# Optimization experiments

Measured on AMD Instinct MI355X. Metric: run time of the kernel, lower is better.

## Reference

```python
import jax, jax.numpy as jnp
import numpy as np

EPS = 1e-12  # tf.math.l2_normalize epsilon

def _l2_normalize(v, axis):
    sq = jnp.sum(v * v, axis=axis, keepdims=True)
    return v * jax.lax.rsqrt(jnp.maximum(sq, EPS))

def setup_inputs() -> dict:
    key = jax.random.key(0)
    k1, k2, k3 = jax.random.split(key, 3)
    B, H, Wd, Cin, K = 16, 64, 64, 512, 64  # K == dim (required by the source's broadcast)
    x = jax.random.normal(k1, (B, H, Wd, Cin), dtype=jnp.float32)
    W = jax.random.normal(k2, (Cin, K), dtype=jnp.float32) * (1.0 / np.sqrt(Cin))
    b = jnp.zeros((K,), dtype=jnp.float32)
    C = jax.random.uniform(k3, (1, 1, 1, K, K), dtype=jnp.float32)  # [1,1,1,dim,clusters]
    return {"x": x, "W": W, "b": b, "C": C}

def reference(x, W, b, C):
    # 1x1 conv: per-pixel linear projection to cluster logits. NOTE: the
    # original code overwrites x with the conv output, so the VLAD residual
    # is built from these logits, not the input features (faithful to source).
    f = jnp.einsum('bhwc,ck->bhwk', x, W) + b            # [B,H,W,K]
    s = jax.nn.softmax(f, axis=-1)                        # soft assignment over clusters
    # a: [B,H,W,1,K], residual: [B,H,W,dim,K] with dim==K
    v = s[..., None, :] * (f[..., :, None] + C)           # [B,H,W,dim,K]
    v = jnp.sum(v, axis=(1, 2))                           # [B,dim,K]
    v = jnp.transpose(v, (0, 2, 1))                       # [B,K,dim]
    # postnorm=True: intra-normalize per cluster, then global L2 of flattened
    v = _l2_normalize(v, axis=-1)
    flat = v.reshape(v.shape[0], -1)                      # [B, K*dim]
    return _l2_normalize(flat, axis=-1)
```

## Files before the change

kernel.cpp:

```cpp
#include <hip/hip_runtime.h>
#include <hip/hip_bf16.h>

#define NB 16
#define HW 4096
#define CIN 512
#define KCL 64
#define BP 64
#define NCHUNK 64
#define PSTRIDE 72

typedef short s16x8 __attribute__((ext_vector_type(8)));
typedef int   i32x4 __attribute__((ext_vector_type(4)));
typedef float f32x4 __attribute__((ext_vector_type(4)));

__device__ __forceinline__ unsigned short f2bf(float f) {
    unsigned u = __builtin_bit_cast(unsigned, f);
    u += 0x7fffu + ((u >> 16) & 1u);
    return (unsigned short)(u >> 16);
}

__device__ __forceinline__ unsigned pk2(float lo, float hi) {
    __hip_bfloat162 h = __float22bfloat162_rn(make_float2(lo, hi));
    unsigned r;
    __builtin_memcpy(&r, &h, 4);
    return r;
}

__global__ void vlad_prep(const float* __restrict__ Wm, float* __restrict__ A_g,
                          unsigned short* __restrict__ Wt_g)
{
    const int i = blockIdx.x * 256 + threadIdx.x;
    if (i < NB * KCL * KCL + NB * KCL) A_g[i] = 0.f;
    if (i < CIN * KCL) {
        const int c = i >> 6;
        const int n = i & 63;
        Wt_g[n * 512 + c] = f2bf(Wm[i]);
    }
}

__global__ __launch_bounds__(256, 4) void vlad_main(
    const float* __restrict__ x, const unsigned short* __restrict__ Wt_g,
    const float* __restrict__ bv, float* __restrict__ A_g,
    float* __restrict__ sumS_g)
{
    __shared__ unsigned short ft[KCL * PSTRIDE];
    __shared__ unsigned short st[KCL * PSTRIDE];

    const int t = threadIdx.x;
    const int b = blockIdx.x >> 6;
    const int chunk = blockIdx.x & 63;
    const int pb = b * HW + chunk * BP;

    const int wid = t >> 6;
    const int lane = t & 63;
    const int col = lane & 15;
    const int g = lane >> 4;
    const int wpix = pb + wid * 16;

    f32x4 acc[4];
#pragma unroll
    for (int nt = 0; nt < 4; ++nt) acc[nt] = (f32x4){0.f, 0.f, 0.f, 0.f};

    const float* xr0 = x + (size_t)(wpix + col) * CIN + g * 8;
    const unsigned short* wbase = Wt_g + col * 512 + g * 8;

#pragma unroll
    for (int kk = 0; kk < 16; ++kk) {
        const int k0 = kk * 32;
        const float4 u00 = *(const float4*)(xr0 + k0);
        const float4 u01 = *(const float4*)(xr0 + k0 + 4);
        s16x8 wf[4];
#pragma unroll
        for (int nt = 0; nt < 4; ++nt)
            wf[nt] = *(const s16x8*)(wbase + nt * (16 * 512) + k0);
        const i32x4 a0i = {(int)pk2(u00.x, u00.y), (int)pk2(u00.z, u00.w),
                           (int)pk2(u01.x, u01.y), (int)pk2(u01.z, u01.w)};
        const s16x8 a0 = __builtin_bit_cast(s16x8, a0i);
#pragma unroll
        for (int nt = 0; nt < 4; ++nt)
            acc[nt] = __builtin_amdgcn_mfma_f32_16x16x32_bf16(a0, wf[nt], acc[nt], 0, 0, 0);
    }

    float bj[4];
#pragma unroll
    for (int nt = 0; nt < 4; ++nt) bj[nt] = bv[nt * 16 + col];
    float ssum[4] = {0.f, 0.f, 0.f, 0.f};
    float fv[4][4], sv[4][4];

#pragma unroll
    for (int r = 0; r < 4; ++r) {
        float v0 = acc[0][r] + bj[0];
        float v1 = acc[1][r] + bj[1];
        float v2 = acc[2][r] + bj[2];
        float v3 = acc[3][r] + bj[3];
        float m = fmaxf(fmaxf(v0, v1), fmaxf(v2, v3));
        m = fmaxf(m, __shfl_xor(m, 1));
        m = fmaxf(m, __shfl_xor(m, 2));
        m = fmaxf(m, __shfl_xor(m, 4));
        m = fmaxf(m, __shfl_xor(m, 8));
        const float e0 = __expf(v0 - m);
        const float e1 = __expf(v1 - m);
        const float e2 = __expf(v2 - m);
        const float e3 = __expf(v3 - m);
        float lsum = e0 + e1 + e2 + e3;
        lsum += __shfl_xor(lsum, 1);
        lsum += __shfl_xor(lsum, 2);
        lsum += __shfl_xor(lsum, 4);
        lsum += __shfl_xor(lsum, 8);
        const float rl = 1.0f / lsum;
        fv[0][r] = v0; fv[1][r] = v1; fv[2][r] = v2; fv[3][r] = v3;
        sv[0][r] = e0 * rl; sv[1][r] = e1 * rl; sv[2][r] = e2 * rl; sv[3][r] = e3 * rl;
        ssum[0] += sv[0][r]; ssum[1] += sv[1][r]; ssum[2] += sv[2][r]; ssum[3] += sv[3][r];
    }

    const int pbase = wid * 16 + g * 4;
#pragma unroll
    for (int nt = 0; nt < 4; ++nt) {
        uint2 fw, sw;
        fw.x = pk2(fv[nt][0], fv[nt][1]); fw.y = pk2(fv[nt][2], fv[nt][3]);
        sw.x = pk2(sv[nt][0], sv[nt][1]); sw.y = pk2(sv[nt][2], sv[nt][3]);
        *(uint2*)(ft + (nt * 16 + col) * PSTRIDE + pbase) = fw;
        *(uint2*)(st + (nt * 16 + col) * PSTRIDE + pbase) = sw;
    }

#pragma unroll
    for (int nt = 0; nt < 4; ++nt) {
        ssum[nt] += __shfl_xor(ssum[nt], 16);
        ssum[nt] += __shfl_xor(ssum[nt], 32);
    }
    if (g == 0) {
#pragma unroll
        for (int nt = 0; nt < 4; ++nt)
            atomicAdd(sumS_g + b * KCL + nt * 16 + col, ssum[nt]);
    }
    __syncthreads();

    f32x4 acc2[4];
#pragma unroll
    for (int nt = 0; nt < 4; ++nt) acc2[nt] = (f32x4){0.f, 0.f, 0.f, 0.f};

    const unsigned short* fta = ft + (wid * 16 + col) * PSTRIDE + g * 8;
#pragma unroll
    for (int kk = 0; kk < 2; ++kk) {
        const s16x8 af = *(const s16x8*)(fta + kk * 32);
#pragma unroll
        for (int nt = 0; nt < 4; ++nt) {
            const s16x8 bf = *(const s16x8*)(st + (nt * 16 + col) * PSTRIDE + kk * 32 + g * 8);
            acc2[nt] = __builtin_amdgcn_mfma_f32_16x16x32_bf16(af, bf, acc2[nt], 0, 0, 0);
        }
    }

    float* Ab = A_g + b * (KCL * KCL);
#pragma unroll
    for (int nt = 0; nt < 4; ++nt)
#pragma unroll
        for (int r = 0; r < 4; ++r)
            atomicAdd(Ab + (wid * 16 + g * 4 + r) * KCL + nt * 16 + col, acc2[nt][r]);
}

__global__ __launch_bounds__(256) void vlad_finalize(
    const float* __restrict__ A_g, const float* __restrict__ sumS_g,
    const float* __restrict__ Cm, float* __restrict__ out)
{
    __shared__ float red[4];
    const int b = blockIdx.x;
    const int t = threadIdx.x;
    const int k = t >> 2;
    const int dg = t & 3;
    const float sS = sumS_g[b * 64 + k];
    float v[16];
    float ssq = 0.f;
#pragma unroll
    for (int i = 0; i < 16; ++i) {
        const int d = dg * 16 + i;
        const float val = A_g[((size_t)b * 64 + d) * 64 + k] + Cm[d * 64 + k] * sS;
        v[i] = val;
        ssq += val * val;
    }
    ssq += __shfl_xor(ssq, 1);
    ssq += __shfl_xor(ssq, 2);
    const float rn = rsqrtf(fmaxf(ssq, 1e-12f));
    float gpart = 0.f;
#pragma unroll
    for (int i = 0; i < 16; ++i) {
        v[i] *= rn;
        gpart += v[i] * v[i];
    }
#pragma unroll
    for (int m = 1; m < 64; m <<= 1) gpart += __shfl_xor(gpart, m);
    if ((t & 63) == 0) red[t >> 6] = gpart;
    __syncthreads();
    const float gsq = red[0] + red[1] + red[2] + red[3];
    const float gr = rsqrtf(fmaxf(gsq, 1e-12f));
    float* o = out + (size_t)b * 4096 + k * 64 + dg * 16;
#pragma unroll
    for (int i = 0; i < 16; ++i) o[i] = v[i] * gr;
}

extern "C" void kernel_launch(void* const* d_in, const int* in_sizes, int n_in,
                              void* d_out, int out_size, void* d_ws, size_t ws_size,
                              hipStream_t stream)
{
    const float* x  = (const float*)d_in[0];
    const float* Wm = (const float*)d_in[1];
    const float* bv = (const float*)d_in[2];
    const float* Cm = (const float*)d_in[3];

    float* A_g = (float*)d_ws;
    float* sumS_g = A_g + NB * KCL * KCL;
    unsigned short* Wt_g = (unsigned short*)(sumS_g + NB * KCL);

    const int nz = NB * KCL * KCL + NB * KCL;
    vlad_prep<<<(nz + 255) / 256, 256, 0, stream>>>(Wm, A_g, Wt_g);
    vlad_main<<<NB * NCHUNK, 256, 0, stream>>>(x, Wt_g, bv, A_g, sumS_g);
    vlad_finalize<<<NB, 256, 0, stream>>>(A_g, sumS_g, Cm, (float*)d_out);
}
```

Before: 223.2 us.

## Stage bf16 weights in LDS and double pixels per block

```diff
diff --git a/kernel.cpp b/kernel.cpp
--- a/kernel.cpp
+++ b/kernel.cpp
@@ -5,9 +5,10 @@
 #define HW 4096
 #define CIN 512
 #define KCL 64
-#define BP 64
-#define NCHUNK 64
-#define PSTRIDE 72
+#define BP 128
+#define NCHUNK 32
+#define PSTR_W 520
+#define PSTR_P 136
 
 typedef short s16x8 __attribute__((ext_vector_type(8)));
 typedef int   i32x4 __attribute__((ext_vector_type(4)));
@@ -38,44 +39,54 @@
     }
 }
 
-__global__ __launch_bounds__(256, 4) void vlad_main(
+__global__ __launch_bounds__(512, 4) void vlad_main(
     const float* __restrict__ x, const unsigned short* __restrict__ Wt_g,
     const float* __restrict__ bv, float* __restrict__ A_g,
     float* __restrict__ sumS_g)
 {
-    __shared__ unsigned short ft[KCL * PSTRIDE];
-    __shared__ unsigned short st[KCL * PSTRIDE];
+    __shared__ unsigned short smem[KCL * PSTR_W];
+    unsigned short* wt = smem;
+    unsigned short* ft = smem;
+    unsigned short* st = smem + KCL * PSTR_P;
 
     const int t = threadIdx.x;
-    const int b = blockIdx.x >> 6;
-    const int chunk = blockIdx.x & 63;
+    const int b = blockIdx.x >> 5;
+    const int chunk = blockIdx.x & 31;
     const int pb = b * HW + chunk * BP;
 
     const int wid = t >> 6;
     const int lane = t & 63;
     const int col = lane & 15;
     const int g = lane >> 4;
-    const int wpix = pb + wid * 16;
+
+#pragma unroll
+    for (int i = 0; i < 8; ++i) {
+        const int idx = i * 512 + t;
+        const int row = idx >> 6;
+        const int c8 = (idx & 63) << 3;
+        *(s16x8*)(wt + row * PSTR_W + c8) = *(const s16x8*)(Wt_g + row * 512 + c8);
+    }
+    __syncthreads();
 
     f32x4 acc[4];
 #pragma unroll
     for (int nt = 0; nt < 4; ++nt) acc[nt] = (f32x4){0.f, 0.f, 0.f, 0.f};
 
-    const float* xr0 = x + (size_t)(wpix + col) * CIN + g * 8;
-    const unsigned short* wbase = Wt_g + col * 512 + g * 8;
+    const float* xr0 = x + (size_t)(pb + wid * 16 + col) * CIN + g * 8;
+    const unsigned short* wb = wt + col * PSTR_W + g * 8;
 
 #pragma unroll
     for (int kk = 0; kk < 16; ++kk) {
         const int k0 = kk * 32;
-        const float4 u00 = *(const float4*)(xr0 + k0);
-        const float4 u01 = *(const float4*)(xr0 + k0 + 4);
+        const float4 u0 = *(const float4*)(xr0 + k0);
+        const float4 u1 = *(const float4*)(xr0 + k0 + 4);
         s16x8 wf[4];
 #pragma unroll
         for (int nt = 0; nt < 4; ++nt)
-            wf[nt] = *(const s16x8*)(wbase + nt * (16 * 512) + k0);
-        const i32x4 a0i = {(int)pk2(u00.x, u00.y), (int)pk2(u00.z, u00.w),
-                           (int)pk2(u01.x, u01.y), (int)pk2(u01.z, u01.w)};
-        const s16x8 a0 = __builtin_bit_cast(s16x8, a0i);
+            wf[nt] = *(const s16x8*)(wb + nt * (16 * PSTR_W) + k0);
+        const i32x4 ai = {(int)pk2(u0.x, u0.y), (int)pk2(u0.z, u0.w),
+                          (int)pk2(u1.x, u1.y), (int)pk2(u1.z, u1.w)};
+        const s16x8 a0 = __builtin_bit_cast(s16x8, ai);
 #pragma unroll
         for (int nt = 0; nt < 4; ++nt)
             acc[nt] = __builtin_amdgcn_mfma_f32_16x16x32_bf16(a0, wf[nt], acc[nt], 0, 0, 0);
@@ -113,14 +124,16 @@
         ssum[0] += sv[0][r]; ssum[1] += sv[1][r]; ssum[2] += sv[2][r]; ssum[3] += sv[3][r];
     }
 
+    __syncthreads();
+
     const int pbase = wid * 16 + g * 4;
 #pragma unroll
     for (int nt = 0; nt < 4; ++nt) {
         uint2 fw, sw;
         fw.x = pk2(fv[nt][0], fv[nt][1]); fw.y = pk2(fv[nt][2], fv[nt][3]);
         sw.x = pk2(sv[nt][0], sv[nt][1]); sw.y = pk2(sv[nt][2], sv[nt][3]);
-        *(uint2*)(ft + (nt * 16 + col) * PSTRIDE + pbase) = fw;
-        *(uint2*)(st + (nt * 16 + col) * PSTRIDE + pbase) = sw;
+        *(uint2*)(ft + (nt * 16 + col) * PSTR_P + pbase) = fw;
+        *(uint2*)(st + (nt * 16 + col) * PSTR_P + pbase) = sw;
     }
 
 #pragma unroll
@@ -135,17 +148,19 @@
     }
     __syncthreads();
 
+    const int dt = wid & 3;
+    const int ph = wid >> 2;
     f32x4 acc2[4];
 #pragma unroll
     for (int nt = 0; nt < 4; ++nt) acc2[nt] = (f32x4){0.f, 0.f, 0.f, 0.f};
 
-    const unsigned short* fta = ft + (wid * 16 + col) * PSTRIDE + g * 8;
+    const unsigned short* fta = ft + (dt * 16 + col) * PSTR_P + ph * 64 + g * 8;
 #pragma unroll
     for (int kk = 0; kk < 2; ++kk) {
         const s16x8 af = *(const s16x8*)(fta + kk * 32);
 #pragma unroll
         for (int nt = 0; nt < 4; ++nt) {
-            const s16x8 bf = *(const s16x8*)(st + (nt * 16 + col) * PSTRIDE + kk * 32 + g * 8);
+            const s16x8 bf = *(const s16x8*)(st + (nt * 16 + col) * PSTR_P + ph * 64 + kk * 32 + g * 8);
             acc2[nt] = __builtin_amdgcn_mfma_f32_16x16x32_bf16(af, bf, acc2[nt], 0, 0, 0);
         }
     }
@@ -155,7 +170,7 @@
     for (int nt = 0; nt < 4; ++nt)
 #pragma unroll
         for (int r = 0; r < 4; ++r)
-            atomicAdd(Ab + (wid * 16 + g * 4 + r) * KCL + nt * 16 + col, acc2[nt][r]);
+            atomicAdd(Ab + (dt * 16 + g * 4 + r) * KCL + nt * 16 + col, acc2[nt][r]);
 }
 
 __global__ __launch_bounds__(256) void vlad_finalize(
@@ -212,6 +227,6 @@
 
     const int nz = NB * KCL * KCL + NB * KCL;
     vlad_prep<<<(nz + 255) / 256, 256, 0, stream>>>(Wm, A_g, Wt_g);
-    vlad_main<<<NB * NCHUNK, 256, 0, stream>>>(x, Wt_g, bv, A_g, sumS_g);
+    vlad_main<<<NB * NCHUNK, 512, 0, stream>>>(x, Wt_g, bv, A_g, sumS_g);
     vlad_finalize<<<NB, 256, 0, stream>>>(A_g, sumS_g, Cm, (float*)d_out);
 }
```

Result: faster. 213.6 us (-4.3%).
